# Optimization experiments

Hardware: AMD Instinct MI355X
Metric: run time of the kernel (lower is better)

The kernel has to match this reference:

```python
import jax, jax.numpy as jnp
import numpy as np

H = 4  # heads (init_kwargs)
E = 64  # embed_size
D = E // H
PREC_DIM = 2
FF = 4 * E


def _layernorm(x, g, b, eps=1e-5):
    mu = jnp.mean(x, axis=-1, keepdims=True)
    var = jnp.mean((x - mu) ** 2, axis=-1, keepdims=True)
    return (x - mu) * jax.lax.rsqrt(var + eps) * g + b


def setup_inputs() -> dict:
    key = jax.random.key(0)
    ks = jax.random.split(key, 16)
    B, S, N = 128, 192, 32
    s = 0.05
    return {
        "precedence": jax.random.normal(ks[0], (B, S, N, PREC_DIM), dtype=jnp.float32),
        "top_mask": jax.random.randint(ks[1], (B, N), 0, 2, dtype=jnp.int32),
        "We": jax.random.normal(ks[2], (PREC_DIM, E), dtype=jnp.float32) * s,
        "be": jnp.zeros((E,), jnp.float32),
        "Wq": jax.random.normal(ks[3], (D, D), dtype=jnp.float32) * s,
        "Wk": jax.random.normal(ks[4], (D, D), dtype=jnp.float32) * s,
        "Wv": jax.random.normal(ks[5], (D, D), dtype=jnp.float32) * s,
        "Wo": jax.random.normal(ks[6], (E, E), dtype=jnp.float32) * s,
        "bo": jnp.zeros((E,), jnp.float32),
        "ln1_g": jnp.ones((E,), jnp.float32),
        "ln1_b": jnp.zeros((E,), jnp.float32),
        "W1": jax.random.normal(ks[7], (E, FF), dtype=jnp.float32) * s,
        "b1": jnp.zeros((FF,), jnp.float32),
        "W2": jax.random.normal(ks[8], (FF, E), dtype=jnp.float32) * s,
        "b2": jnp.zeros((E,), jnp.float32),
        "ln2_g": jnp.ones((E,), jnp.float32),
        "ln2_b": jnp.zeros((E,), jnp.float32),
    }


def reference(precedence, top_mask, We, be, Wq, Wk, Wv, Wo, bo,
              ln1_g, ln1_b, W1, b1, W2, b2, ln2_g, ln2_b):
    B, S, N, _ = precedence.shape
    M = B * S
    # embedding: [B,S,N,E]
    pv = precedence @ We + be
    # gather-indexed query: prec_vecs[:, s, s % box_num]
    sidx = jnp.arange(S)
    q = pv[:, sidx, sidx % N]                      # [B,S,E]
    vals = pv.reshape(M, N, E)                     # values == keys
    qr = q.reshape(M, 1, E)
    # mask: [B,1,1,N] expanded over states -> [M,1,1,N]
    mask = jnp.broadcast_to(top_mask[:, None, None, None, :], (B, S, 1, 1, N)).reshape(M, 1, 1, N)
    # per-head linear projections (shared across heads)
    vh = vals.reshape(M, N, H, D) @ Wv
    kh = vals.reshape(M, N, H, D) @ Wk
    qh = qr.reshape(M, 1, H, D) @ Wq
    energy = jnp.einsum("mqhd,mkhd->mhqk", qh, kh)           # [M,H,1,N]
    energy = jnp.where(mask == 0, jnp.float32(-1e20), energy)
    attn = jax.nn.softmax(energy / jnp.sqrt(jnp.float32(E)), axis=-1)
    oh = jnp.einsum("mhqk,mkhd->mqhd", attn, vh).reshape(M, 1, E)
    ao = oh @ Wo + bo
    x = _layernorm(ao + qr, ln1_g, ln1_b)
    ff = jax.nn.relu(x @ W1 + b1) @ W2 + b2
    out = _layernorm(ff + x, ln2_g, ln2_b)
    return out.reshape(B, S, E)
```

## Files before the change

kernel.cpp:

```cpp
#include <hip/hip_runtime.h>
#include <math.h>

namespace {

constexpr int S_  = 192;
constexpr int TPP = 8;
constexpr int PPB = 2;

__device__ __forceinline__ void wave_fence() {
  asm volatile("s_waitcnt lgkmcnt(0)" ::: "memory");
}

__launch_bounds__(256)
__attribute__((amdgpu_waves_per_eu(6, 8)))
__global__ void prec_fused(
    const float* __restrict__ prec,  const int*   __restrict__ tmask,
    const float* __restrict__ We,    const float* __restrict__ be,
    const float* __restrict__ Wq,    const float* __restrict__ Wk,
    const float* __restrict__ Wv,    const float* __restrict__ Wo,
    const float* __restrict__ bo,    const float* __restrict__ g1,
    const float* __restrict__ bb1,   const float* __restrict__ W1,
    const float* __restrict__ b1,    const float* __restrict__ W2,
    const float* __restrict__ b2,    const float* __restrict__ g2,
    const float* __restrict__ bb2,   float* __restrict__ out)
{
  __shared__ __align__(16) float sh[PPB][2048];
  __shared__ __align__(16) float sxoh[PPB][TPP][64];

  const int tid   = threadIdx.x;
  const int wv    = tid >> 6;
  const int pairL = wv >> 1;
  const int w2    = wv & 1;
  const int lane  = tid & 63;
  const int u     = lane >> 5;
  const int n     = lane & 31;
  const int pairbase = (blockIdx.x * PPB + pairL) * TPP;
  const int bidx0 = pairbase / S_;
  const int srow0 = pairbase - bidx0 * S_;

  float* __restrict__ sc = &sh[0][0];

  if (tid < 64) { sc[tid] = We[tid]; sc[64 + tid] = We[64 + tid]; sc[128 + tid] = be[tid]; }
  sc[192 + tid] = Wq[tid];
  sc[448 + tid] = Wk[tid];
  sc[704 + tid] = Wv[tid];
  __syncthreads();

  {
    const int sel = wv;
    if (sel < 3) {
      const int h = (tid >> 4) & 3, c = tid & 15;
      const float* Wm = sc + 192 + sel * 256;
      float a0 = 0.f, a1 = 0.f, a2 = 0.f;
      #pragma unroll
      for (int dp = 0; dp < 16; ++dp) {
        const float w = Wm[dp * 16 + c];
        a0 = fmaf(sc[h * 16 + dp],       w, a0);
        a1 = fmaf(sc[64 + h * 16 + dp],  w, a1);
        a2 = fmaf(sc[128 + h * 16 + dp], w, a2);
      }
      const int base = 960 + sel * 192 + h * 48 + c;
      sc[base] = a0; sc[base + 16] = a1; sc[base + 32] = a2;
    }
  }
  __syncthreads();

  if (tid < 36) {
    const int h = tid / 9, ab = tid - h * 9, a = ab / 3, b = ab - a * 3;
    const float* Tp = sc + 960  + h * 48 + a * 16;
    const float* Kp = sc + 1152 + h * 48 + b * 16;
    float s = 0.f;
    #pragma unroll
    for (int c = 0; c < 16; ++c) s = fmaf(Tp[c], Kp[c], s);
    sc[1536 + tid] = s;
  }
  {
    const int e = tid & 63, h = wv;
    const float* Vp = sc + 1344 + h * 48;
    float q0 = 0.f, q1 = 0.f, q2 = 0.f;
    #pragma unroll
    for (int dp = 0; dp < 16; ++dp) {
      const float wo = Wo[(h * 16 + dp) * 64 + e];
      q0 = fmaf(Vp[dp],      wo, q0);
      q1 = fmaf(Vp[16 + dp], wo, q1);
      q2 = fmaf(Vp[32 + dp], wo, q2);
    }
    sc[1600 + (h * 3 + 0) * 64 + e] = q0;
    sc[1600 + (h * 3 + 1) * 64 + e] = q1;
    sc[1600 + (h * 3 + 2) * 64 + e] = q2;
  }
  __syncthreads();

  float m0[9], m1[9];
  #pragma unroll
  for (int i = 0; i < 9; ++i) {
    m0[i] = sc[1536 + (2 * u) * 9 + i];
    m1[i] = sc[1536 + (2 * u + 1) * 9 + i];
  }
  const int hoA = 2 * u, hoB = 2 * u + 1, htA = 2 - 2 * u, htB = 3 - 2 * u;
  float gO0[2], gO1[2], gT0[2], gT1[2];
  #pragma unroll
  for (int a = 0; a < 2; ++a) {
    gO0[a] = sc[1600 + (hoA * 3 + a) * 64 + lane];
    gO1[a] = sc[1600 + (hoB * 3 + a) * 64 + lane];
    gT0[a] = sc[1600 + (htA * 3 + a) * 64 + lane];
    gT1[a] = sc[1600 + (htB * 3 + a) * 64 + lane];
  }
  float c0 = bo[lane];
  #pragma unroll
  for (int h = 0; h < 4; ++h) c0 += sc[1600 + (h * 3 + 2) * 64 + lane];
  const float we0l = sc[lane], we1l = sc[64 + lane], bel = sc[128 + lane];
  const float g1l = g1[lane], b1l_ = bb1[lane];
  const bool masked = (tmask[bidx0 * 32 + n] == 0);
  const bool allm   = (__all((int)masked) != 0);
  __syncthreads();

  #pragma unroll 2
  for (int p = 0; p < 4; ++p) {
    const int tl    = w2 * 4 + p;
    const int m     = pairbase + tl;
    const int nstar = (srow0 + tl) & 31;

    const float qx = prec[(size_t)m * 64 + nstar * 2];
    const float qy = prec[(size_t)m * 64 + nstar * 2 + 1];
    const float2 pin = *(const float2*)(prec + (size_t)m * 64 + n * 2);

    const float cA0 = fmaf(qy, m0[3], fmaf(qx, m0[0], m0[6]));
    const float cB0 = fmaf(qy, m0[4], fmaf(qx, m0[1], m0[7]));
    const float cC0 = fmaf(qy, m0[5], fmaf(qx, m0[2], m0[8]));
    const float cA1 = fmaf(qy, m1[3], fmaf(qx, m1[0], m1[6]));
    const float cB1 = fmaf(qy, m1[4], fmaf(qx, m1[1], m1[7]));
    const float cC1 = fmaf(qy, m1[5], fmaf(qx, m1[2], m1[8]));
    const float en0 = fmaf(pin.y, cB0, fmaf(pin.x, cA0, cC0)) * 0.125f;
    const float en1 = fmaf(pin.y, cB1, fmaf(pin.x, cA1, cC1)) * 0.125f;

    float pe0, pe1;
    if (allm) { pe0 = 1.f; pe1 = 1.f; }
    else {
      pe0 = masked ? 0.f : __expf(en0);
      pe1 = masked ? 0.f : __expf(en1);
    }

    float r0 = pe0 * pin.x, r1 = pe0 * pin.y, r2 = pe0;
    float r3 = pe1 * pin.x, r4 = pe1 * pin.y, r5 = pe1;
    #pragma unroll
    for (int o = 1; o < 32; o <<= 1) {
      r0 += __shfl_xor(r0, o, 64); r1 += __shfl_xor(r1, o, 64);
      r2 += __shfl_xor(r2, o, 64); r3 += __shfl_xor(r3, o, 64);
      r4 += __shfl_xor(r4, o, 64); r5 += __shfl_xor(r5, o, 64);
    }
    const float o0 = __shfl_xor(r0, 32, 64), o1 = __shfl_xor(r1, 32, 64);
    const float o2 = __shfl_xor(r2, 32, 64), o3 = __shfl_xor(r3, 32, 64);
    const float o4 = __shfl_xor(r4, 32, 64), o5 = __shfl_xor(r5, 32, 64);
    const float i0 = __builtin_amdgcn_rcpf(r2), i1 = __builtin_amdgcn_rcpf(r5);
    const float i2 = __builtin_amdgcn_rcpf(o2), i3 = __builtin_amdgcn_rcpf(o5);

    float v = c0;
    v = fmaf(fmaf(r1, gO0[1], r0 * gO0[0]), i0, v);
    v = fmaf(fmaf(r4, gO1[1], r3 * gO1[0]), i1, v);
    v = fmaf(fmaf(o1, gT0[1], o0 * gT0[0]), i2, v);
    v = fmaf(fmaf(o4, gT1[1], o3 * gT1[0]), i3, v);
    v += fmaf(qy, we1l, fmaf(qx, we0l, bel));

    float sm = v, s2 = v * v;
    #pragma unroll
    for (int o = 1; o < 64; o <<= 1) {
      sm += __shfl_xor(sm, o, 64);
      s2 += __shfl_xor(s2, o, 64);
    }
    const float mu  = sm * (1.f / 64.f);
    const float var = s2 * (1.f / 64.f) - mu * mu;
    const float rs  = rsqrtf(var + 1e-5f);
    sxoh[pairL][tl][lane] = (v - mu) * rs * g1l + b1l_;
  }
  __syncthreads();

  const int c2 = 128 * w2 + 2 * lane;
  float hacc[TPP][2];
  {
    const float2 b1v = *(const float2*)(b1 + c2);
    #pragma unroll
    for (int t = 0; t < TPP; ++t) { hacc[t][0] = b1v.x; hacc[t][1] = b1v.y; }
  }
  #pragma unroll 4
  for (int e4 = 0; e4 < 16; ++e4) {
    float2 wr[4];
    #pragma unroll
    for (int kk = 0; kk < 4; ++kk)
      wr[kk] = *(const float2*)(W1 + (e4 * 4 + kk) * 256 + c2);
    #pragma unroll
    for (int t = 0; t < TPP; ++t) {
      const float4 xv = *(const float4*)&sxoh[pairL][t][e4 * 4];
      hacc[t][0] = fmaf(xv.x, wr[0].x, hacc[t][0]);
      hacc[t][1] = fmaf(xv.x, wr[0].y, hacc[t][1]);
      hacc[t][0] = fmaf(xv.y, wr[1].x, hacc[t][0]);
      hacc[t][1] = fmaf(xv.y, wr[1].y, hacc[t][1]);
      hacc[t][0] = fmaf(xv.z, wr[2].x, hacc[t][0]);
      hacc[t][1] = fmaf(xv.z, wr[2].y, hacc[t][1]);
      hacc[t][0] = fmaf(xv.w, wr[3].x, hacc[t][0]);
      hacc[t][1] = fmaf(xv.w, wr[3].y, hacc[t][1]);
    }
  }
  float* __restrict__ h1buf = sh[pairL];
  #pragma unroll
  for (int t = 0; t < TPP; ++t) {
    float2 hv;
    hv.x = fmaxf(hacc[t][0], 0.f);
    hv.y = fmaxf(hacc[t][1], 0.f);
    *(float2*)&h1buf[t * 256 + c2] = hv;
  }
  wave_fence();

  float f2[TPP];
  #pragma unroll
  for (int t = 0; t < TPP; ++t) f2[t] = 0.f;
  #pragma unroll 4
  for (int k = 0; k < 32; ++k) {
    const int f4 = 32 * w2 + k;
    const float w0 = W2[(f4 * 4 + 0) * 64 + lane];
    const float w1 = W2[(f4 * 4 + 1) * 64 + lane];
    const float w2_ = W2[(f4 * 4 + 2) * 64 + lane];
    const float w3 = W2[(f4 * 4 + 3) * 64 + lane];
    #pragma unroll
    for (int t = 0; t < TPP; ++t) {
      const float4 hv = *(const float4*)&h1buf[t * 256 + f4 * 4];
      f2[t] = fmaf(hv.x, w0, f2[t]);
      f2[t] = fmaf(hv.y, w1, f2[t]);
      f2[t] = fmaf(hv.z, w2_, f2[t]);
      f2[t] = fmaf(hv.w, w3, f2[t]);
    }
  }
  __syncthreads();

  float* __restrict__ fpart = h1buf;
  {
    const int tb = (1 - w2) * 4;
    #pragma unroll
    for (int i = 0; i < 4; ++i)
      fpart[(tb + i) * 64 + lane] = f2[tb + i];
  }
  __syncthreads();

  {
    const float b2l = b2[lane], g2l = g2[lane], bb2l = bb2[lane];
    #pragma unroll 2
    for (int i = 0; i < 4; ++i) {
      const int tl = w2 * 4 + i;
      const float v = f2[tl] + fpart[tl * 64 + lane] + b2l + sxoh[pairL][tl][lane];
      float sm = v, s2 = v * v;
      #pragma unroll
      for (int o = 1; o < 64; o <<= 1) {
        sm += __shfl_xor(sm, o, 64);
        s2 += __shfl_xor(s2, o, 64);
      }
      const float mu  = sm * (1.f / 64.f);
      const float var = s2 * (1.f / 64.f) - mu * mu;
      const float rs  = rsqrtf(var + 1e-5f);
      out[(size_t)(pairbase + tl) * 64 + lane] = (v - mu) * rs * g2l + bb2l;
    }
  }
}

}

extern "C" void kernel_launch(void* const* d_in, const int* in_sizes, int n_in,
                              void* d_out, int out_size, void* d_ws, size_t ws_size,
                              hipStream_t stream) {
  (void)in_sizes; (void)n_in; (void)d_ws; (void)ws_size; (void)out_size;
  const float* prec = (const float*)d_in[0];
  const int*   tm   = (const int*)  d_in[1];
  const float* We   = (const float*)d_in[2];
  const float* be   = (const float*)d_in[3];
  const float* Wq   = (const float*)d_in[4];
  const float* Wk   = (const float*)d_in[5];
  const float* Wv   = (const float*)d_in[6];
  const float* Wo   = (const float*)d_in[7];
  const float* bo   = (const float*)d_in[8];
  const float* g1   = (const float*)d_in[9];
  const float* bb1  = (const float*)d_in[10];
  const float* W1   = (const float*)d_in[11];
  const float* b1   = (const float*)d_in[12];
  const float* W2   = (const float*)d_in[13];
  const float* b2   = (const float*)d_in[14];
  const float* g2   = (const float*)d_in[15];
  const float* bb2  = (const float*)d_in[16];

  dim3 grid(1536), block(256);
  hipLaunchKernelGGL(prec_fused, grid, block, 0, stream,
                     prec, tm, We, be, Wq, Wk, Wv, Wo, bo, g1, bb1,
                     W1, b1, W2, b2, g2, bb2, (float*)d_out);
}
```

Baseline: 133.7 us.

## Retile FFN matmuls with wider register tiles and use DPP for shuffle reductions

Replaces the first two butterfly steps of each cross-lane reduction with DPP quad-permute adds instead of ds_swizzle/bpermute shuffles. The FFN first layer is retiled so each lane computes a 4x4 (rows x columns) block using float4 W1 loads, and the second layer splits the K dimension across half-waves with float2 W2 loads, combining halves with a shuffle. The final partial-sum exchange moves to a dedicated shared buffer, removing one block barrier, and LayerNorm 2 processes two elements per lane with float2 stores. The aim is more register reuse per LDS and global load, at the cost of more shared memory and a different register footprint.

Result: faster. 130.8 us (-2.2%).

```diff
diff --git a/kernel.cpp b/kernel.cpp
--- a/kernel.cpp
+++ b/kernel.cpp
@@ -9,6 +9,14 @@
 
 __device__ __forceinline__ void wave_fence() {
   asm volatile("s_waitcnt lgkmcnt(0)" ::: "memory");
+}
+__device__ __forceinline__ float dpp_xor1_add(float x) {
+  return x + __int_as_float(__builtin_amdgcn_update_dpp(
+      0, __float_as_int(x), 0xB1, 0xF, 0xF, true));
+}
+__device__ __forceinline__ float dpp_xor2_add(float x) {
+  return x + __int_as_float(__builtin_amdgcn_update_dpp(
+      0, __float_as_int(x), 0x4E, 0xF, 0xF, true));
 }
 
 __launch_bounds__(256)
@@ -26,6 +34,7 @@
 {
   __shared__ __align__(16) float sh[PPB][2048];
   __shared__ __align__(16) float sxoh[PPB][TPP][64];
+  __shared__ __align__(16) float sfp[PPB][TPP][64];
 
   const int tid   = threadIdx.x;
   const int wv    = tid >> 6;
@@ -46,22 +55,19 @@
   sc[704 + tid] = Wv[tid];
   __syncthreads();
 
-  {
-    const int sel = wv;
-    if (sel < 3) {
-      const int h = (tid >> 4) & 3, c = tid & 15;
-      const float* Wm = sc + 192 + sel * 256;
-      float a0 = 0.f, a1 = 0.f, a2 = 0.f;
-      #pragma unroll
-      for (int dp = 0; dp < 16; ++dp) {
-        const float w = Wm[dp * 16 + c];
-        a0 = fmaf(sc[h * 16 + dp],       w, a0);
-        a1 = fmaf(sc[64 + h * 16 + dp],  w, a1);
-        a2 = fmaf(sc[128 + h * 16 + dp], w, a2);
-      }
-      const int base = 960 + sel * 192 + h * 48 + c;
-      sc[base] = a0; sc[base + 16] = a1; sc[base + 32] = a2;
-    }
+  if (wv < 3) {
+    const int h = (tid >> 4) & 3, cc = tid & 15;
+    const float* Wm = sc + 192 + wv * 256;
+    float a0 = 0.f, a1 = 0.f, a2 = 0.f;
+    #pragma unroll
+    for (int dp = 0; dp < 16; ++dp) {
+      const float w = Wm[dp * 16 + cc];
+      a0 = fmaf(sc[h * 16 + dp],       w, a0);
+      a1 = fmaf(sc[64 + h * 16 + dp],  w, a1);
+      a2 = fmaf(sc[128 + h * 16 + dp], w, a2);
+    }
+    const int base = 960 + wv * 192 + h * 48 + cc;
+    sc[base] = a0; sc[base + 16] = a1; sc[base + 32] = a2;
   }
   __syncthreads();
 
@@ -71,7 +77,7 @@
     const float* Kp = sc + 1152 + h * 48 + b * 16;
     float s = 0.f;
     #pragma unroll
-    for (int c = 0; c < 16; ++c) s = fmaf(Tp[c], Kp[c], s);
+    for (int cc = 0; cc < 16; ++cc) s = fmaf(Tp[cc], Kp[cc], s);
     sc[1536 + tid] = s;
   }
   {
@@ -143,8 +149,12 @@
 
     float r0 = pe0 * pin.x, r1 = pe0 * pin.y, r2 = pe0;
     float r3 = pe1 * pin.x, r4 = pe1 * pin.y, r5 = pe1;
-    #pragma unroll
-    for (int o = 1; o < 32; o <<= 1) {
+    r0 = dpp_xor1_add(r0); r1 = dpp_xor1_add(r1); r2 = dpp_xor1_add(r2);
+    r3 = dpp_xor1_add(r3); r4 = dpp_xor1_add(r4); r5 = dpp_xor1_add(r5);
+    r0 = dpp_xor2_add(r0); r1 = dpp_xor2_add(r1); r2 = dpp_xor2_add(r2);
+    r3 = dpp_xor2_add(r3); r4 = dpp_xor2_add(r4); r5 = dpp_xor2_add(r5);
+    #pragma unroll
+    for (int o = 4; o < 32; o <<= 1) {
       r0 += __shfl_xor(r0, o, 64); r1 += __shfl_xor(r1, o, 64);
       r2 += __shfl_xor(r2, o, 64); r3 += __shfl_xor(r3, o, 64);
       r4 += __shfl_xor(r4, o, 64); r5 += __shfl_xor(r5, o, 64);
@@ -163,8 +173,10 @@
     v += fmaf(qy, we1l, fmaf(qx, we0l, bel));
 
     float sm = v, s2 = v * v;
-    #pragma unroll
-    for (int o = 1; o < 64; o <<= 1) {
+    sm = dpp_xor1_add(sm); s2 = dpp_xor1_add(s2);
+    sm = dpp_xor2_add(sm); s2 = dpp_xor2_add(s2);
+    #pragma unroll
+    for (int o = 4; o < 64; o <<= 1) {
       sm += __shfl_xor(sm, o, 64);
       s2 += __shfl_xor(s2, o, 64);
     }
@@ -175,88 +187,126 @@
   }
   __syncthreads();
 
-  const int c2 = 128 * w2 + 2 * lane;
-  float hacc[TPP][2];
+  const int q  = lane >> 5;
+  const int l5 = lane & 31;
+  const int F0 = 128 * w2;
+
+  const int c = F0 + 4 * l5;
+  float hacc[4][4];
   {
-    const float2 b1v = *(const float2*)(b1 + c2);
-    #pragma unroll
-    for (int t = 0; t < TPP; ++t) { hacc[t][0] = b1v.x; hacc[t][1] = b1v.y; }
+    const float4 b1v = *(const float4*)(b1 + c);
+    #pragma unroll
+    for (int p = 0; p < 4; ++p) {
+      hacc[p][0] = b1v.x; hacc[p][1] = b1v.y; hacc[p][2] = b1v.z; hacc[p][3] = b1v.w;
+    }
   }
   #pragma unroll 4
   for (int e4 = 0; e4 < 16; ++e4) {
-    float2 wr[4];
-    #pragma unroll
-    for (int kk = 0; kk < 4; ++kk)
-      wr[kk] = *(const float2*)(W1 + (e4 * 4 + kk) * 256 + c2);
-    #pragma unroll
-    for (int t = 0; t < TPP; ++t) {
-      const float4 xv = *(const float4*)&sxoh[pairL][t][e4 * 4];
-      hacc[t][0] = fmaf(xv.x, wr[0].x, hacc[t][0]);
-      hacc[t][1] = fmaf(xv.x, wr[0].y, hacc[t][1]);
-      hacc[t][0] = fmaf(xv.y, wr[1].x, hacc[t][0]);
-      hacc[t][1] = fmaf(xv.y, wr[1].y, hacc[t][1]);
-      hacc[t][0] = fmaf(xv.z, wr[2].x, hacc[t][0]);
-      hacc[t][1] = fmaf(xv.z, wr[2].y, hacc[t][1]);
-      hacc[t][0] = fmaf(xv.w, wr[3].x, hacc[t][0]);
-      hacc[t][1] = fmaf(xv.w, wr[3].y, hacc[t][1]);
+    float4 w1r[4];
+    #pragma unroll
+    for (int j = 0; j < 4; ++j)
+      w1r[j] = *(const float4*)(W1 + (e4 * 4 + j) * 256 + c);
+    #pragma unroll
+    for (int p = 0; p < 4; ++p) {
+      const float4 xv = *(const float4*)&sxoh[pairL][4 * q + p][e4 * 4];
+      hacc[p][0] = fmaf(xv.x, w1r[0].x, hacc[p][0]);
+      hacc[p][1] = fmaf(xv.x, w1r[0].y, hacc[p][1]);
+      hacc[p][2] = fmaf(xv.x, w1r[0].z, hacc[p][2]);
+      hacc[p][3] = fmaf(xv.x, w1r[0].w, hacc[p][3]);
+      hacc[p][0] = fmaf(xv.y, w1r[1].x, hacc[p][0]);
+      hacc[p][1] = fmaf(xv.y, w1r[1].y, hacc[p][1]);
+      hacc[p][2] = fmaf(xv.y, w1r[1].z, hacc[p][2]);
+      hacc[p][3] = fmaf(xv.y, w1r[1].w, hacc[p][3]);
+      hacc[p][0] = fmaf(xv.z, w1r[2].x, hacc[p][0]);
+      hacc[p][1] = fmaf(xv.z, w1r[2].y, hacc[p][1]);
+      hacc[p][2] = fmaf(xv.z, w1r[2].z, hacc[p][2]);
+      hacc[p][3] = fmaf(xv.z, w1r[2].w, hacc[p][3]);
+      hacc[p][0] = fmaf(xv.w, w1r[3].x, hacc[p][0]);
+      hacc[p][1] = fmaf(xv.w, w1r[3].y, hacc[p][1]);
+      hacc[p][2] = fmaf(xv.w, w1r[3].z, hacc[p][2]);
+      hacc[p][3] = fmaf(xv.w, w1r[3].w, hacc[p][3]);
     }
   }
   float* __restrict__ h1buf = sh[pairL];
   #pragma unroll
-  for (int t = 0; t < TPP; ++t) {
-    float2 hv;
-    hv.x = fmaxf(hacc[t][0], 0.f);
-    hv.y = fmaxf(hacc[t][1], 0.f);
-    *(float2*)&h1buf[t * 256 + c2] = hv;
+  for (int p = 0; p < 4; ++p) {
+    float4 hv;
+    hv.x = fmaxf(hacc[p][0], 0.f); hv.y = fmaxf(hacc[p][1], 0.f);
+    hv.z = fmaxf(hacc[p][2], 0.f); hv.w = fmaxf(hacc[p][3], 0.f);
+    *(float4*)&h1buf[(4 * q + p) * 256 + c] = hv;
   }
   wave_fence();
 
-  float f2[TPP];
-  #pragma unroll
-  for (int t = 0; t < TPP; ++t) f2[t] = 0.f;
+  const int e0 = 2 * l5;
+  const int f4base = 32 * w2 + 16 * q;
+  float2 f2a[8];
+  #pragma unroll
+  for (int t = 0; t < 8; ++t) { f2a[t].x = 0.f; f2a[t].y = 0.f; }
   #pragma unroll 4
-  for (int k = 0; k < 32; ++k) {
-    const int f4 = 32 * w2 + k;
-    const float w0 = W2[(f4 * 4 + 0) * 64 + lane];
-    const float w1 = W2[(f4 * 4 + 1) * 64 + lane];
-    const float w2_ = W2[(f4 * 4 + 2) * 64 + lane];
-    const float w3 = W2[(f4 * 4 + 3) * 64 + lane];
-    #pragma unroll
-    for (int t = 0; t < TPP; ++t) {
+  for (int k = 0; k < 16; ++k) {
+    const int f4 = f4base + k;
+    float2 w2r[4];
+    #pragma unroll
+    for (int j = 0; j < 4; ++j)
+      w2r[j] = *(const float2*)(W2 + (f4 * 4 + j) * 64 + e0);
+    #pragma unroll
+    for (int t = 0; t < 8; ++t) {
       const float4 hv = *(const float4*)&h1buf[t * 256 + f4 * 4];
-      f2[t] = fmaf(hv.x, w0, f2[t]);
-      f2[t] = fmaf(hv.y, w1, f2[t]);
-      f2[t] = fmaf(hv.z, w2_, f2[t]);
-      f2[t] = fmaf(hv.w, w3, f2[t]);
-    }
-  }
-  __syncthreads();
-
-  float* __restrict__ fpart = h1buf;
+      f2a[t].x = fmaf(hv.x, w2r[0].x, f2a[t].x);
+      f2a[t].y = fmaf(hv.x, w2r[0].y, f2a[t].y);
+      f2a[t].x = fmaf(hv.y, w2r[1].x, f2a[t].x);
+      f2a[t].y = fmaf(hv.y, w2r[1].y, f2a[t].y);
+      f2a[t].x = fmaf(hv.z, w2r[2].x, f2a[t].x);
+      f2a[t].y = fmaf(hv.z, w2r[2].y, f2a[t].y);
+      f2a[t].x = fmaf(hv.w, w2r[3].x, f2a[t].x);
+      f2a[t].y = fmaf(hv.w, w2r[3].y, f2a[t].y);
+    }
+  }
+  #pragma unroll
+  for (int t = 0; t < 8; ++t) {
+    f2a[t].x += __shfl_xor(f2a[t].x, 32, 64);
+    f2a[t].y += __shfl_xor(f2a[t].y, 32, 64);
+  }
+  if (lane < 32) {
+    if (w2 == 0) {
+      #pragma unroll
+      for (int i = 0; i < 4; ++i) *(float2*)&sfp[pairL][4 + i][e0] = f2a[4 + i];
+    } else {
+      #pragma unroll
+      for (int i = 0; i < 4; ++i) *(float2*)&sfp[pairL][i][e0] = f2a[i];
+    }
+  }
+  __syncthreads();
+
   {
-    const int tb = (1 - w2) * 4;
-    #pragma unroll
-    for (int i = 0; i < 4; ++i)
-      fpart[(tb + i) * 64 + lane] = f2[tb + i];
-  }
-  __syncthreads();
-
-  {
-    const float b2l = b2[lane], g2l = g2[lane], bb2l = bb2[lane];
-    #pragma unroll 2
-    for (int i = 0; i < 4; ++i) {
-      const int tl = w2 * 4 + i;
-      const float v = f2[tl] + fpart[tl * 64 + lane] + b2l + sxoh[pairL][tl][lane];
-      float sm = v, s2 = v * v;
+    const float2 b2v  = *(const float2*)(b2 + e0);
+    const float2 g2v  = *(const float2*)(g2 + e0);
+    const float2 bb2v = *(const float2*)(bb2 + e0);
+    #pragma unroll
+    for (int i = 0; i < 2; ++i) {
+      float2 mine;
+      if (w2 == 0) mine = q ? f2a[2 + i] : f2a[i];
+      else         mine = q ? f2a[6 + i] : f2a[4 + i];
+      const int tl = w2 * 4 + 2 * q + i;
+      const float2 fp = *(const float2*)&sfp[pairL][tl][e0];
+      const float2 xr = *(const float2*)&sxoh[pairL][tl][e0];
+      const float v0 = mine.x + fp.x + b2v.x + xr.x;
+      const float v1 = mine.y + fp.y + b2v.y + xr.y;
+      float sm = v0 + v1, s2v = v0 * v0 + v1 * v1;
+      sm = dpp_xor1_add(sm); s2v = dpp_xor1_add(s2v);
+      sm = dpp_xor2_add(sm); s2v = dpp_xor2_add(s2v);
       #pragma unroll
-      for (int o = 1; o < 64; o <<= 1) {
-        sm += __shfl_xor(sm, o, 64);
-        s2 += __shfl_xor(s2, o, 64);
+      for (int o = 4; o < 32; o <<= 1) {
+        sm  += __shfl_xor(sm, o, 64);
+        s2v += __shfl_xor(s2v, o, 64);
       }
       const float mu  = sm * (1.f / 64.f);
-      const float var = s2 * (1.f / 64.f) - mu * mu;
+      const float var = s2v * (1.f / 64.f) - mu * mu;
       const float rs  = rsqrtf(var + 1e-5f);
-      out[(size_t)(pairbase + tl) * 64 + lane] = (v - mu) * rs * g2l + bb2l;
+      float2 o2;
+      o2.x = (v0 - mu) * rs * g2v.x + bb2v.x;
+      o2.y = (v1 - mu) * rs * g2v.y + bb2v.y;
+      *(float2*)(out + (size_t)(pairbase + tl) * 64 + e0) = o2;
     }
   }
 }
```
